# Optimization experiments

Measured on AMD Instinct MI355X. Metric: run time of the kernel, lower is better.

The kernel has to match this reference:

```python
import jax, jax.numpy as jnp
import numpy as np

T, B, I, H = 2048, 4096, 3, 5  # seq_len, batch, input_size, hidden_size (from module)


def setup_inputs() -> dict:
    key = jax.random.key(0)
    ks = jax.random.split(key, 10)
    k = 1.0 / np.sqrt(H)  # torch nn.RNN default init bound
    u = lambda kk, shape: jax.random.uniform(kk, shape, jnp.float32, -k, k)
    return {
        "x": jax.random.normal(ks[0], (T, B, I), jnp.float32),
        "hx": jax.random.normal(ks[1], (2, B, H), jnp.float32),
        "w_ih0": u(ks[2], (H, I)),
        "w_hh0": u(ks[3], (H, H)),
        "b_ih0": u(ks[4], (H,)),
        "b_hh0": u(ks[5], (H,)),
        "w_ih1": u(ks[6], (H, H)),
        "w_hh1": u(ks[7], (H, H)),
        "b_ih1": u(ks[8], (H,)),
        "b_hh1": u(ks[9], (H,)),
    }


def reference(x, hx, w_ih0, w_hh0, b_ih0, b_hh0, w_ih1, w_hh1, b_ih1, b_hh1):
    # Precompute layer-0 input projections for all timesteps in one big GEMM.
    pre0 = jnp.einsum("tbi,hi->tbh", x, w_ih0) + b_ih0  # [T, B, H]

    def step(carry, p0_t):
        h0, h1 = carry
        h0 = jnp.tanh(p0_t + h0 @ w_hh0.T + b_hh0)
        h1 = jnp.tanh(h0 @ w_ih1.T + b_ih1 + h1 @ w_hh1.T + b_hh1)
        return (h0, h1), h1

    (h0_f, h1_f), out = jax.lax.scan(step, (hx[0], hx[1]), pre0)
    h_n = jnp.stack([h0_f, h1_f])  # [2, B, H]
    return out, h_n
```

## Files before the change

### kernel.cpp

```cpp
#include <hip/hip_runtime.h>


#define SEQ_T 2048
#define BATCH 4096
#define ISZ 3
#define HSZ 5
#define KB 8
#define NBLK (SEQ_T / KB)

template<int K>
__device__ __forceinline__ float bcastk(float v) {
    return __int_as_float(__builtin_amdgcn_ds_swizzle(__float_as_int(v), (K << 5) | 0x18));
}

__device__ __forceinline__ float tanh_fast(float a) {
    float e = __builtin_amdgcn_exp2f(a);
    return fmaf(-2.0f, __builtin_amdgcn_rcpf(1.0f + e), 1.0f);
}

__global__ __launch_bounds__(256, 1)
void rnn2_lanes(const float* __restrict__ x, const float* __restrict__ hx,
                const float* __restrict__ w_ih0, const float* __restrict__ w_hh0,
                const float* __restrict__ b_ih0, const float* __restrict__ b_hh0,
                const float* __restrict__ w_ih1, const float* __restrict__ w_hh1,
                const float* __restrict__ b_ih1, const float* __restrict__ b_hh1,
                float* __restrict__ out)
{
    const int tid  = threadIdx.x;
    const int gthr = blockIdx.x * 256 + tid;
    const int c    = gthr >> 3;
    const int sub  = tid & 7;
    const int j    = (sub < HSZ) ? sub : (HSZ - 1);
    const float S  = 2.8853900817779268f;

    float wi0[ISZ], wh0[HSZ], wi1[HSZ], wh1[HSZ];
    const float bias0 = S * (b_ih0[j] + b_hh0[j]);
    const float bias1 = S * (b_ih1[j] + b_hh1[j]);
#pragma unroll
    for (int i = 0; i < ISZ; i++) wi0[i] = S * w_ih0[j * ISZ + i];
#pragma unroll
    for (int k = 0; k < HSZ; k++) {
        wh0[k] = S * w_hh0[j * HSZ + k];
        wi1[k] = S * w_ih1[j * HSZ + k];
        wh1[k] = S * w_hh1[j * HSZ + k];
    }

    float h0b[HSZ], h1b[HSZ];
#pragma unroll
    for (int k = 0; k < HSZ; k++) {
        h0b[k] = hx[(size_t)c * HSZ + k];
        h1b[k] = hx[(size_t)BATCH * HSZ + (size_t)c * HSZ + k];
    }

    const float* xp = x + (size_t)c * ISZ;
    float xbuf[KB][ISZ];
#pragma unroll
    for (int tt = 0; tt < KB; tt++)
#pragma unroll
        for (int i = 0; i < ISZ; i++)
            xbuf[tt][i] = xp[(size_t)tt * BATCH * ISZ + i];

    float* opv = out + (size_t)c * HSZ + j;

    for (int blk = 0; blk < NBLK; blk++) {
        const int pf = (blk + 1 < NBLK) ? (blk + 1) * KB : blk * KB;
#pragma unroll
        for (int tt = 0; tt < KB; tt++) {
            const float xv0 = xbuf[tt][0], xv1 = xbuf[tt][1], xv2 = xbuf[tt][2];
            const float* xq = xp + (size_t)(pf + tt) * BATCH * ISZ;
            xbuf[tt][0] = xq[0]; xbuf[tt][1] = xq[1]; xbuf[tt][2] = xq[2];

            float a = bias0, cc = 0.0f;
            a  = fmaf(xv0,    wi0[0], a);
            cc = fmaf(xv1,    wi0[1], cc);
            a  = fmaf(xv2,    wi0[2], a);
            cc = fmaf(h0b[0], wh0[0], cc);
            a  = fmaf(h0b[1], wh0[1], a);
            cc = fmaf(h0b[2], wh0[2], cc);
            a  = fmaf(h0b[3], wh0[3], a);
            cc = fmaf(h0b[4], wh0[4], cc);
            a += cc;
            const float h0n = tanh_fast(a);

            h0b[0] = bcastk<0>(h0n);
            h0b[1] = bcastk<1>(h0n);
            h0b[2] = bcastk<2>(h0n);
            h0b[3] = bcastk<3>(h0n);
            h0b[4] = bcastk<4>(h0n);

            float d = bias1, ee = 0.0f;
            d  = fmaf(h0b[0], wi1[0], d);
            ee = fmaf(h0b[1], wi1[1], ee);
            d  = fmaf(h0b[2], wi1[2], d);
            ee = fmaf(h0b[3], wi1[3], ee);
            d  = fmaf(h0b[4], wi1[4], d);
            ee = fmaf(h1b[0], wh1[0], ee);
            d  = fmaf(h1b[1], wh1[1], d);
            ee = fmaf(h1b[2], wh1[2], ee);
            d  = fmaf(h1b[3], wh1[3], d);
            ee = fmaf(h1b[4], wh1[4], ee);
            d += ee;
            const float h1n = tanh_fast(d);

            *opv = h1n;
            opv += (size_t)BATCH * HSZ;

            h1b[0] = bcastk<0>(h1n);
            h1b[1] = bcastk<1>(h1n);
            h1b[2] = bcastk<2>(h1n);
            h1b[3] = bcastk<3>(h1n);
            h1b[4] = bcastk<4>(h1n);
        }
    }

    float* hn = out + (size_t)SEQ_T * BATCH * HSZ;
    const float h0f = (j == 0) ? h0b[0] : (j == 1) ? h0b[1] :
                      (j == 2) ? h0b[2] : (j == 3) ? h0b[3] : h0b[4];
    const float h1f = (j == 0) ? h1b[0] : (j == 1) ? h1b[1] :
                      (j == 2) ? h1b[2] : (j == 3) ? h1b[3] : h1b[4];
    hn[(size_t)c * HSZ + j] = h0f;
    hn[(size_t)BATCH * HSZ + (size_t)c * HSZ + j] = h1f;
}

extern "C" void kernel_launch(void* const* d_in, const int* in_sizes, int n_in,
                              void* d_out, int out_size, void* d_ws, size_t ws_size,
                              hipStream_t stream) {
    rnn2_lanes<<<(BATCH * 8) / 256, 256, 0, stream>>>(
        (const float*)d_in[0], (const float*)d_in[1],
        (const float*)d_in[2], (const float*)d_in[3],
        (const float*)d_in[4], (const float*)d_in[5],
        (const float*)d_in[6], (const float*)d_in[7],
        (const float*)d_in[8], (const float*)d_in[9],
        (float*)d_out);
}
```

Measured before the change: 480.6 us.

## Map each batch row to a lane quad with packed FMAs and DPP broadcasts

Each batch row now runs on 4 lanes instead of 8. Every lane computes its own hidden unit and also the fifth unit, using 2-wide vector FMAs (packed fp32). The cross-lane broadcast moves from ds_swizzle to a DPP quad_perm mov, which has lower latency, and the fifth value stays local. Launch becomes 64-thread blocks and the x prefetch depth doubles to 16. This halves the lanes per row and shortens the per-step serial dependency chain, at the cost of duplicated work on the fifth unit, more registers, and every lane redundantly writing h_n.

```diff
diff --git a/kernel.cpp b/kernel.cpp
--- a/kernel.cpp
+++ b/kernel.cpp
@@ -1,16 +1,19 @@
 #include <hip/hip_runtime.h>
 
+
+typedef float v2f __attribute__((ext_vector_type(2)));
 
 #define SEQ_T 2048
 #define BATCH 4096
 #define ISZ 3
 #define HSZ 5
-#define KB 8
+#define KB 16
 #define NBLK (SEQ_T / KB)
 
 template<int K>
-__device__ __forceinline__ float bcastk(float v) {
-    return __int_as_float(__builtin_amdgcn_ds_swizzle(__float_as_int(v), (K << 5) | 0x18));
+__device__ __forceinline__ float qbcast(float v) {
+    return __int_as_float(__builtin_amdgcn_mov_dpp(
+        __float_as_int(v), K * 0x55, 0xF, 0xF, false));
 }
 
 __device__ __forceinline__ float tanh_fast(float a) {
@@ -18,31 +21,35 @@
     return fmaf(-2.0f, __builtin_amdgcn_rcpf(1.0f + e), 1.0f);
 }
 
-__global__ __launch_bounds__(256, 1)
-void rnn2_lanes(const float* __restrict__ x, const float* __restrict__ hx,
-                const float* __restrict__ w_ih0, const float* __restrict__ w_hh0,
-                const float* __restrict__ b_ih0, const float* __restrict__ b_hh0,
-                const float* __restrict__ w_ih1, const float* __restrict__ w_hh1,
-                const float* __restrict__ b_ih1, const float* __restrict__ b_hh1,
-                float* __restrict__ out)
+__device__ __forceinline__ v2f vsplat(float s) { return (v2f){s, s}; }
+__device__ __forceinline__ v2f vfma(float s, v2f w, v2f a) {
+    return __builtin_elementwise_fma(vsplat(s), w, a);
+}
+
+__global__ __launch_bounds__(64, 1)
+void rnn2_quad(const float* __restrict__ x, const float* __restrict__ hx,
+               const float* __restrict__ w_ih0, const float* __restrict__ w_hh0,
+               const float* __restrict__ b_ih0, const float* __restrict__ b_hh0,
+               const float* __restrict__ w_ih1, const float* __restrict__ w_hh1,
+               const float* __restrict__ b_ih1, const float* __restrict__ b_hh1,
+               float* __restrict__ out)
 {
-    const int tid  = threadIdx.x;
-    const int gthr = blockIdx.x * 256 + tid;
-    const int c    = gthr >> 3;
-    const int sub  = tid & 7;
-    const int j    = (sub < HSZ) ? sub : (HSZ - 1);
-    const float S  = 2.8853900817779268f;
+    const int tid = threadIdx.x;
+    const int c   = (blockIdx.x * 64 + tid) >> 2;
+    const int ja  = tid & 3;
+    const float S = 2.8853900817779268f;
 
-    float wi0[ISZ], wh0[HSZ], wi1[HSZ], wh1[HSZ];
-    const float bias0 = S * (b_ih0[j] + b_hh0[j]);
-    const float bias1 = S * (b_ih1[j] + b_hh1[j]);
+    v2f wi0p[ISZ], wh0p[HSZ], wi1p[HSZ], wh1p[HSZ];
+    const v2f bias0p = (v2f){ S * (b_ih0[ja] + b_hh0[ja]), S * (b_ih0[4] + b_hh0[4]) };
+    const v2f bias1p = (v2f){ S * (b_ih1[ja] + b_hh1[ja]), S * (b_ih1[4] + b_hh1[4]) };
 #pragma unroll
-    for (int i = 0; i < ISZ; i++) wi0[i] = S * w_ih0[j * ISZ + i];
+    for (int i = 0; i < ISZ; i++)
+        wi0p[i] = (v2f){ S * w_ih0[ja * ISZ + i], S * w_ih0[4 * ISZ + i] };
 #pragma unroll
     for (int k = 0; k < HSZ; k++) {
-        wh0[k] = S * w_hh0[j * HSZ + k];
-        wi1[k] = S * w_ih1[j * HSZ + k];
-        wh1[k] = S * w_hh1[j * HSZ + k];
+        wh0p[k] = (v2f){ S * w_hh0[ja * HSZ + k], S * w_hh0[4 * HSZ + k] };
+        wi1p[k] = (v2f){ S * w_ih1[ja * HSZ + k], S * w_ih1[4 * HSZ + k] };
+        wh1p[k] = (v2f){ S * w_hh1[ja * HSZ + k], S * w_hh1[4 * HSZ + k] };
     }
 
     float h0b[HSZ], h1b[HSZ];
@@ -60,7 +67,8 @@
         for (int i = 0; i < ISZ; i++)
             xbuf[tt][i] = xp[(size_t)tt * BATCH * ISZ + i];
 
-    float* opv = out + (size_t)c * HSZ + j;
+    float* opA = out + (size_t)c * HSZ + ja;
+    float* opB = out + (size_t)c * HSZ + 4;
 
     for (int blk = 0; blk < NBLK; blk++) {
         const int pf = (blk + 1 < NBLK) ? (blk + 1) * KB : blk * KB;
@@ -70,62 +78,65 @@
             const float* xq = xp + (size_t)(pf + tt) * BATCH * ISZ;
             xbuf[tt][0] = xq[0]; xbuf[tt][1] = xq[1]; xbuf[tt][2] = xq[2];
 
-            float a = bias0, cc = 0.0f;
-            a  = fmaf(xv0,    wi0[0], a);
-            cc = fmaf(xv1,    wi0[1], cc);
-            a  = fmaf(xv2,    wi0[2], a);
-            cc = fmaf(h0b[0], wh0[0], cc);
-            a  = fmaf(h0b[1], wh0[1], a);
-            cc = fmaf(h0b[2], wh0[2], cc);
-            a  = fmaf(h0b[3], wh0[3], a);
-            cc = fmaf(h0b[4], wh0[4], cc);
-            a += cc;
-            const float h0n = tanh_fast(a);
+            v2f a = bias0p, cc = (v2f){0.0f, 0.0f};
+            a  = vfma(xv0,    wi0p[0], a);
+            cc = vfma(xv1,    wi0p[1], cc);
+            a  = vfma(xv2,    wi0p[2], a);
+            cc = vfma(h0b[0], wh0p[0], cc);
+            a  = vfma(h0b[1], wh0p[1], a);
+            cc = vfma(h0b[2], wh0p[2], cc);
+            a  = vfma(h0b[3], wh0p[3], a);
+            cc = vfma(h0b[4], wh0p[4], cc);
+            a = a + cc;
+            const float h0nA = tanh_fast(a.x);
+            const float h0nB = tanh_fast(a.y);
 
-            h0b[0] = bcastk<0>(h0n);
-            h0b[1] = bcastk<1>(h0n);
-            h0b[2] = bcastk<2>(h0n);
-            h0b[3] = bcastk<3>(h0n);
-            h0b[4] = bcastk<4>(h0n);
+            h0b[0] = qbcast<0>(h0nA);
+            h0b[1] = qbcast<1>(h0nA);
+            h0b[2] = qbcast<2>(h0nA);
+            h0b[3] = qbcast<3>(h0nA);
+            h0b[4] = h0nB;
 
-            float d = bias1, ee = 0.0f;
-            d  = fmaf(h0b[0], wi1[0], d);
-            ee = fmaf(h0b[1], wi1[1], ee);
-            d  = fmaf(h0b[2], wi1[2], d);
-            ee = fmaf(h0b[3], wi1[3], ee);
-            d  = fmaf(h0b[4], wi1[4], d);
-            ee = fmaf(h1b[0], wh1[0], ee);
-            d  = fmaf(h1b[1], wh1[1], d);
-            ee = fmaf(h1b[2], wh1[2], ee);
-            d  = fmaf(h1b[3], wh1[3], d);
-            ee = fmaf(h1b[4], wh1[4], ee);
-            d += ee;
-            const float h1n = tanh_fast(d);
+            v2f d = bias1p, ee = (v2f){0.0f, 0.0f};
+            d  = vfma(h0b[0], wi1p[0], d);
+            ee = vfma(h0b[1], wi1p[1], ee);
+            d  = vfma(h0b[2], wi1p[2], d);
+            ee = vfma(h0b[3], wi1p[3], ee);
+            d  = vfma(h0b[4], wi1p[4], d);
+            ee = vfma(h1b[0], wh1p[0], ee);
+            d  = vfma(h1b[1], wh1p[1], d);
+            ee = vfma(h1b[2], wh1p[2], ee);
+            d  = vfma(h1b[3], wh1p[3], d);
+            ee = vfma(h1b[4], wh1p[4], ee);
+            d = d + ee;
+            const float h1nA = tanh_fast(d.x);
+            const float h1nB = tanh_fast(d.y);
 
-            *opv = h1n;
-            opv += (size_t)BATCH * HSZ;
+            *opA = h1nA;
+            *opB = h1nB;
+            opA += (size_t)BATCH * HSZ;
+            opB += (size_t)BATCH * HSZ;
 
-            h1b[0] = bcastk<0>(h1n);
-            h1b[1] = bcastk<1>(h1n);
-            h1b[2] = bcastk<2>(h1n);
-            h1b[3] = bcastk<3>(h1n);
-            h1b[4] = bcastk<4>(h1n);
+            h1b[0] = qbcast<0>(h1nA);
+            h1b[1] = qbcast<1>(h1nA);
+            h1b[2] = qbcast<2>(h1nA);
+            h1b[3] = qbcast<3>(h1nA);
+            h1b[4] = h1nB;
         }
     }
 
     float* hn = out + (size_t)SEQ_T * BATCH * HSZ;
-    const float h0f = (j == 0) ? h0b[0] : (j == 1) ? h0b[1] :
-                      (j == 2) ? h0b[2] : (j == 3) ? h0b[3] : h0b[4];
-    const float h1f = (j == 0) ? h1b[0] : (j == 1) ? h1b[1] :
-                      (j == 2) ? h1b[2] : (j == 3) ? h1b[3] : h1b[4];
-    hn[(size_t)c * HSZ + j] = h0f;
-    hn[(size_t)BATCH * HSZ + (size_t)c * HSZ + j] = h1f;
+#pragma unroll
+    for (int k = 0; k < HSZ; k++) {
+        hn[(size_t)c * HSZ + k] = h0b[k];
+        hn[(size_t)BATCH * HSZ + (size_t)c * HSZ + k] = h1b[k];
+    }
 }
 
 extern "C" void kernel_launch(void* const* d_in, const int* in_sizes, int n_in,
                               void* d_out, int out_size, void* d_ws, size_t ws_size,
                               hipStream_t stream) {
-    rnn2_lanes<<<(BATCH * 8) / 256, 256, 0, stream>>>(
+    rnn2_quad<<<(BATCH * 4) / 64, 64, 0, stream>>>(
         (const float*)d_in[0], (const float*)d_in[1],
         (const float*)d_in[2], (const float*)d_in[3],
         (const float*)d_in[4], (const float*)d_in[5],
```

Result: no change. 487.4 us (+1.4%).
